# Performance work log

Hardware: AMD Instinct MI355X
Metric: run time of the kernel (lower is better)

Reference implementation:

```python
import jax, jax.numpy as jnp
import numpy as np

H = 12  # num_heads


def rotate_half(x):
    x1, x2 = jnp.split(x, 2, axis=-1)
    return jnp.concatenate([-x2, x1], axis=-1)


def setup_inputs() -> dict:
    key = jax.random.key(0)
    ks = jax.random.split(key, 8)
    B, N, C = 4, 2048, 768
    num_special = 5
    Ns = N - num_special
    D = C // H
    x = jax.random.normal(ks[0], (B, N, C), dtype=jnp.float32)
    rope_cos = jax.random.uniform(ks[1], (Ns, D), dtype=jnp.float32)
    rope_sin = jax.random.uniform(ks[2], (Ns, D), dtype=jnp.float32)
    W_qkv = jax.random.normal(ks[3], (C, 3 * C), dtype=jnp.float32) * (C ** -0.5)
    b_qkv = jax.random.normal(ks[4], (3 * C,), dtype=jnp.float32) * 0.02
    W_proj = jax.random.normal(ks[5], (C, C), dtype=jnp.float32) * (C ** -0.5)
    b_proj = jax.random.normal(ks[6], (C,), dtype=jnp.float32) * 0.02
    return {"x": x, "rope_cos": rope_cos, "rope_sin": rope_sin,
            "W_qkv": W_qkv, "b_qkv": b_qkv, "W_proj": W_proj, "b_proj": b_proj,
            "num_special": num_special}


def reference(x, rope_cos, rope_sin, W_qkv, b_qkv, W_proj, b_proj, num_special):
    B, N, C = x.shape
    D = C // H
    scale = D ** -0.5
    qkv = (x @ W_qkv + b_qkv).reshape(B, N, 3, H, D)
    qkv = jnp.transpose(qkv, (2, 0, 3, 1, 4))  # [3, B, H, N, D]
    q, k, v = qkv[0], qkv[1], qkv[2]
    # partial RoPE: special tokens untouched, spatial tokens rotated
    q_spec, q_spat = q[:, :, :num_special], q[:, :, num_special:]
    k_spec, k_spat = k[:, :, :num_special], k[:, :, num_special:]
    q_spat = q_spat * rope_cos + rotate_half(q_spat) * rope_sin
    k_spat = k_spat * rope_cos + rotate_half(k_spat) * rope_sin
    q = jnp.concatenate([q_spec, q_spat], axis=2)
    k = jnp.concatenate([k_spec, k_spat], axis=2)
    attn = jnp.einsum('bhqd,bhkd->bhqk', q, k) * scale  # [B,H,N,N]
    attn = jax.nn.softmax(attn, axis=-1)
    out = jnp.einsum('bhqk,bhkd->bhqd', attn, v)  # [B,H,N,D]
    out = jnp.transpose(out, (0, 2, 1, 3)).reshape(B, N, C)
    return out @ W_proj + b_proj
```

## Files before the change

kernel.cpp:

```cpp
#include <hip/hip_runtime.h>
#include <stdint.h>

typedef unsigned short u16;
typedef __bf16 bf16x8 __attribute__((ext_vector_type(8)));
typedef short s16x4 __attribute__((ext_vector_type(4)));
typedef float f32x4 __attribute__((ext_vector_type(4)));

typedef __attribute__((address_space(1))) void gvoid_t;
typedef __attribute__((address_space(3))) void lvoid_t;

struct alignas(16) U128 { uint32_t x, y, z, w; };
struct alignas(16) F128 { float x, y, z, w; };
struct alignas(8)  U64v { uint32_t x, y; };

__device__ __forceinline__ void gld16(const u16* g, u16* lds) {
  __builtin_amdgcn_global_load_lds((gvoid_t*)const_cast<u16*>(g),
                                   (lvoid_t*)lds, 16, 0, 0);
}

__device__ __forceinline__ u16 f2bf(float f) {
  uint32_t u = __builtin_bit_cast(uint32_t, f);
  u += 0x7FFFu + ((u >> 16) & 1u);
  return (u16)(u >> 16);
}
__device__ __forceinline__ float bf2f(u16 h) {
  return __builtin_bit_cast(float, (uint32_t)h << 16);
}
__device__ __forceinline__ bf16x8 ldfrag(const u16* p) {
  U128 u = *reinterpret_cast<const U128*>(p);
  return __builtin_bit_cast(bf16x8, u);
}
__device__ __forceinline__ uint32_t pkbf(float a, float b) {
  uint32_t ua = __builtin_bit_cast(uint32_t, a) + 0x8000u;
  uint32_t ub = __builtin_bit_cast(uint32_t, b) + 0x8000u;
  return (ua >> 16) | (ub & 0xFFFF0000u);
}

__device__ __forceinline__ float EXP2(float x) { return __builtin_amdgcn_exp2f(x); }

__global__ void cvt_f32_bf16(const float* __restrict__ in, u16* __restrict__ out) {
  int i = (blockIdx.x * 256 + threadIdx.x) * 4;
  F128 v = *reinterpret_cast<const F128*>(in + i);
  U64v o;
  o.x = (uint32_t)f2bf(v.x) | ((uint32_t)f2bf(v.y) << 16);
  o.y = (uint32_t)f2bf(v.z) | ((uint32_t)f2bf(v.w) << 16);
  *reinterpret_cast<U64v*>(out + i) = o;
}

__global__ void transpose_cvt(const float* __restrict__ W, u16* __restrict__ Wt,
                              int K, int N) {
  __shared__ float T[32][33];
  const int n0 = blockIdx.x * 32, k0 = blockIdx.y * 32;
  const int tid = threadIdx.x;
#pragma unroll
  for (int i = 0; i < 4; ++i) {
    int e = i * 256 + tid, r = e >> 5, c = e & 31;
    T[r][c] = W[(size_t)(k0 + r) * N + n0 + c];
  }
  __syncthreads();
#pragma unroll
  for (int i = 0; i < 4; ++i) {
    int e = i * 256 + tid, r = e >> 5, c = e & 31;
    Wt[(size_t)(n0 + r) * K + k0 + c] = f2bf(T[c][r]);
  }
}

__global__ __launch_bounds__(256, 2)
void gemm_bt(const u16* __restrict__ A, const u16* __restrict__ Bt,
             const float* __restrict__ bias, float* __restrict__ C,
             int M, int N, int K) {
  __shared__ u16 As[128 * 32];
  __shared__ u16 Bs[128 * 32];
  const int tid = threadIdx.x;
  const int wave = tid >> 6, lane = tid & 63;
  const int quad = lane >> 4, l16 = lane & 15;
  const int m0 = blockIdx.y * 128, n0 = blockIdx.x * 128;
  const int wr = (wave & 1) * 64, wc = (wave >> 1) * 64;

  f32x4 acc[4][4];
#pragma unroll
  for (int i = 0; i < 4; ++i)
#pragma unroll
    for (int j = 0; j < 4; ++j) acc[i][j] = (f32x4){0.f, 0.f, 0.f, 0.f};

  for (int k0 = 0; k0 < K; k0 += 32) {
    __syncthreads();
#pragma unroll
    for (int j = 0; j < 2; ++j) {
      int c = (wave * 2 + j) * 64 + lane;
      int row = c >> 2, kq = c & 3;
      gld16(A + (size_t)(m0 + row) * K + k0 + kq * 8, &As[(wave * 2 + j) * 512]);
      gld16(Bt + (size_t)(n0 + row) * K + k0 + kq * 8, &Bs[(wave * 2 + j) * 512]);
    }
    __syncthreads();
    bf16x8 af[4], bfr[4];
#pragma unroll
    for (int rb = 0; rb < 4; ++rb) af[rb] = ldfrag(&As[(wr + rb * 16 + l16) * 32 + quad * 8]);
#pragma unroll
    for (int cb = 0; cb < 4; ++cb) bfr[cb] = ldfrag(&Bs[(wc + cb * 16 + l16) * 32 + quad * 8]);
#pragma unroll
    for (int rb = 0; rb < 4; ++rb)
#pragma unroll
      for (int cb = 0; cb < 4; ++cb)
        acc[rb][cb] = __builtin_amdgcn_mfma_f32_16x16x32_bf16(af[rb], bfr[cb], acc[rb][cb], 0, 0, 0);
  }
#pragma unroll
  for (int cb = 0; cb < 4; ++cb) {
    int col = n0 + wc + cb * 16 + l16;
    float bv = bias[col];
#pragma unroll
    for (int rb = 0; rb < 4; ++rb) {
#pragma unroll
      for (int r = 0; r < 4; ++r) {
        int row = m0 + wr + rb * 16 + quad * 4 + r;
        C[(size_t)row * N + col] = acc[rb][cb][r] + bv;
      }
    }
  }
}

__global__ __launch_bounds__(256, 2)
void gemm_qkv_rope(const u16* __restrict__ A, const u16* __restrict__ Bt,
                   const float* __restrict__ bias,
                   const float* __restrict__ cosT, const float* __restrict__ sinT,
                   const int* __restrict__ nsp,
                   u16* __restrict__ Qo, u16* __restrict__ Ko, u16* __restrict__ Vto) {
  __shared__ u16 As[128 * 32];
  __shared__ u16 Bs[128 * 32];
  const int K = 768, N = 2304;
  const int tid = threadIdx.x;
  const int wave = tid >> 6, lane = tid & 63;
  const int quad = lane >> 4, l16 = lane & 15;
  const int m0 = blockIdx.y * 128, n0 = blockIdx.x * 128;
  const int wr = (wave & 1) * 64, wc = (wave >> 1) * 64;

  f32x4 acc[4][4];
#pragma unroll
  for (int i = 0; i < 4; ++i)
#pragma unroll
    for (int j = 0; j < 4; ++j) acc[i][j] = (f32x4){0.f, 0.f, 0.f, 0.f};

  for (int k0 = 0; k0 < K; k0 += 32) {
    __syncthreads();
#pragma unroll
    for (int j = 0; j < 2; ++j) {
      int c = (wave * 2 + j) * 64 + lane;
      int row = c >> 2, kq = c & 3;
      gld16(A + (size_t)(m0 + row) * K + k0 + kq * 8, &As[(wave * 2 + j) * 512]);
      gld16(Bt + (size_t)(n0 + row) * K + k0 + kq * 8, &Bs[(wave * 2 + j) * 512]);
    }
    __syncthreads();
    bf16x8 af[4], bfr[4];
#pragma unroll
    for (int rb = 0; rb < 4; ++rb) af[rb] = ldfrag(&As[(wr + rb * 16 + l16) * 32 + quad * 8]);
#pragma unroll
    for (int cb = 0; cb < 4; ++cb) bfr[cb] = ldfrag(&Bs[(wc + cb * 16 + l16) * 32 + quad * 8]);
#pragma unroll
    for (int rb = 0; rb < 4; ++rb)
#pragma unroll
      for (int cb = 0; cb < 4; ++cb)
        acc[rb][cb] = __builtin_amdgcn_mfma_f32_16x16x32_bf16(af[rb], bfr[cb], acc[rb][cb], 0, 0, 0);
  }

  const int sec = blockIdx.x / 6;
  const int gcol0 = n0 + wc;
  const int hh = (gcol0 >> 6) % 12;
  const int bb = m0 >> 11;
  const int nbase = m0 & 2047;
  const int bh = bb * 12 + hh;
  const int num_special = nsp[0];
  const float QS = 0.125f * 1.4426950408889634f;

  if (sec < 2) {
    u16* outp = sec ? Ko : Qo;
    const float qs = sec ? 1.0f : QS;
#pragma unroll
    for (int cbp = 0; cbp < 2; ++cbp) {
      const int d1 = cbp * 16 + l16;
      const int d2 = d1 + 32;
      const float bv1 = bias[gcol0 + d1];
      const float bv2 = bias[gcol0 + d2];
#pragma unroll
      for (int rb = 0; rb < 4; ++rb) {
#pragma unroll
        for (int r = 0; r < 4; ++r) {
          const int n = nbase + wr + rb * 16 + quad * 4 + r;
          float v1 = acc[rb][cbp][r] + bv1;
          float v2 = acc[rb][cbp + 2][r] + bv2;
          float o1, o2;
          if (n < num_special) {
            o1 = v1; o2 = v2;
          } else {
            int ns = n - num_special;
            float c1 = cosT[ns * 64 + d1], s1 = sinT[ns * 64 + d1];
            float c2 = cosT[ns * 64 + d2], s2 = sinT[ns * 64 + d2];
            o1 = v1 * c1 - v2 * s1;
            o2 = v2 * c2 + v1 * s2;
          }
          size_t ob = ((size_t)bh * 2048 + n) * 64;
          outp[ob + d1] = f2bf(o1 * qs);
          outp[ob + d2] = f2bf(o2 * qs);
        }
      }
    }
  } else {
#pragma unroll
    for (int cb = 0; cb < 4; ++cb) {
      const int d = cb * 16 + l16;
      const float bv = bias[gcol0 + d];
#pragma unroll
      for (int rb = 0; rb < 4; ++rb) {
        const int nr = nbase + wr + rb * 16 + quad * 4;
        U64v o;
        o.x = (uint32_t)f2bf(acc[rb][cb][0] + bv) |
              ((uint32_t)f2bf(acc[rb][cb][1] + bv) << 16);
        o.y = (uint32_t)f2bf(acc[rb][cb][2] + bv) |
              ((uint32_t)f2bf(acc[rb][cb][3] + bv) << 16);
        *(U64v*)&Vto[((size_t)bh * 64 + d) * 2048 + nr] = o;
      }
    }
  }
}

__global__ __launch_bounds__(256, 3)
void attn(const u16* __restrict__ Q, const u16* __restrict__ Kg,
          const u16* __restrict__ Vt, u16* __restrict__ Out) {
  __shared__ u16 smem[2 * 64 * 72];
  __shared__ float invS[64];
  u16* Ks = smem;
  u16* Vs = smem + 64 * 72;
  u16* Qs = smem;
  const int tid = threadIdx.x;
  const int wave = tid >> 6, lane = tid & 63;
  const int quad = lane >> 4, l16 = lane & 15;
  const int idx = blockIdx.x;
  const int bh = idx % 48, qt = idx / 48;
  const int b = bh / 12, h = bh % 12;
  const u16* Qb = Q + (size_t)bh * 2048 * 64;
  const u16* Kb = Kg + (size_t)bh * 2048 * 64;
  const u16* Vb = Vt + (size_t)bh * 64 * 2048;
  const int wkey0 = wave * 16;

#pragma unroll
  for (int j = 0; j < 2; ++j) {
    int c = j * 256 + tid;
    int row = c >> 3, kq = c & 7;
    *(U128*)&Qs[row * 72 + kq * 8] =
        *(const U128*)(Qb + (size_t)(qt * 64 + row) * 64 + kq * 8);
  }
  __syncthreads();
  bf16x8 qf[4][2];
#pragma unroll
  for (int m = 0; m < 4; ++m) {
    qf[m][0] = ldfrag(&Qs[(m * 16 + l16) * 72 + quad * 8]);
    qf[m][1] = ldfrag(&Qs[(m * 16 + l16) * 72 + quad * 8 + 32]);
  }

  f32x4 oacc[4][4];
#pragma unroll
  for (int m = 0; m < 4; ++m)
#pragma unroll
    for (int db = 0; db < 4; ++db) oacc[m][db] = (f32x4){0.f, 0.f, 0.f, 0.f};
  float psum[4] = {0.f, 0.f, 0.f, 0.f};

  for (int kt = 0; kt < 32; ++kt) {
    __syncthreads();
#pragma unroll
    for (int j = 0; j < 2; ++j) {
      int c = j * 256 + tid;
      int row = c >> 3, kq = c & 7;
      *(U128*)&Ks[row * 72 + kq * 8] =
          *(const U128*)(Kb + (size_t)(kt * 64 + row) * 64 + kq * 8);
      *(U128*)&Vs[row * 72 + kq * 8] =
          *(const U128*)(Vb + (size_t)row * 2048 + kt * 64 + kq * 8);
    }
    __syncthreads();

    bf16x8 ka0 = ldfrag(&Ks[(wkey0 + l16) * 72 + quad * 8]);
    bf16x8 ka1 = ldfrag(&Ks[(wkey0 + l16) * 72 + quad * 8 + 32]);

    s16x4 pf[4];
#pragma unroll
    for (int m = 0; m < 4; ++m) {
      f32x4 st = (f32x4){0.f, 0.f, 0.f, 0.f};
      st = __builtin_amdgcn_mfma_f32_16x16x32_bf16(ka0, qf[m][0], st, 0, 0, 0);
      st = __builtin_amdgcn_mfma_f32_16x16x32_bf16(ka1, qf[m][1], st, 0, 0, 0);
      float p0 = EXP2(st[0]);
      float p1 = EXP2(st[1]);
      float p2 = EXP2(st[2]);
      float p3 = EXP2(st[3]);
      psum[m] += (p0 + p1) + (p2 + p3);
      U64v pd;
      pd.x = pkbf(p0, p1);
      pd.y = pkbf(p2, p3);
      pf[m] = __builtin_bit_cast(s16x4, pd);
    }

#pragma unroll
    for (int db = 0; db < 4; ++db) {
      s16x4 vf = __builtin_bit_cast(s16x4,
          *(const U64v*)&Vs[(db * 16 + l16) * 72 + wkey0 + quad * 4]);
#pragma unroll
      for (int m = 0; m < 4; ++m)
        oacc[m][db] = __builtin_amdgcn_mfma_f32_16x16x16bf16_1k(pf[m], vf, oacc[m][db], 0, 0, 0);
    }
  }

#pragma unroll
  for (int m = 0; m < 4; ++m) {
    psum[m] += __shfl_xor(psum[m], 16, 64);
    psum[m] += __shfl_xor(psum[m], 32, 64);
  }
  __syncthreads();
  float* LS = (float*)smem;
  if (quad == 0) {
#pragma unroll
    for (int m = 0; m < 4; ++m) LS[wave * 64 + m * 16 + l16] = psum[m];
  }
  __syncthreads();
  if (tid < 64) {
    float tot = LS[tid] + LS[64 + tid] + LS[128 + tid] + LS[192 + tid];
    invS[tid] = 1.0f / tot;
  }

  float* OR = (float*)smem;
  const int q = tid >> 2;
  const int d0 = (tid & 3) * 4;
  const size_t obase = ((size_t)(b * 2048 + qt * 64 + q)) * 768 + h * 64 + d0;
#pragma unroll
  for (int db = 0; db < 4; ++db) {
    __syncthreads();
#pragma unroll
    for (int m = 0; m < 4; ++m)
#pragma unroll
      for (int r = 0; r < 4; ++r)
        OR[(wave * 64 + m * 16 + quad * 4 + r) * 18 + l16] = oacc[m][db][r];
    __syncthreads();
    float s0 = 0.f, s1 = 0.f, s2 = 0.f, s3 = 0.f;
#pragma unroll
    for (int w = 0; w < 4; ++w) {
      const float* p = &OR[(w * 64 + q) * 18 + d0];
      s0 += p[0]; s1 += p[1]; s2 += p[2]; s3 += p[3];
    }
    float iv = invS[q];
    U64v o;
    o.x = (uint32_t)f2bf(s0 * iv) | ((uint32_t)f2bf(s1 * iv) << 16);
    o.y = (uint32_t)f2bf(s2 * iv) | ((uint32_t)f2bf(s3 * iv) << 16);
    *(U64v*)&Out[obase + db * 16] = o;
  }
}

extern "C" void kernel_launch(void* const* d_in, const int* in_sizes, int n_in,
                              void* d_out, int out_size, void* d_ws, size_t ws_size,
                              hipStream_t stream) {
  (void)in_sizes; (void)n_in; (void)out_size; (void)ws_size;
  const float* x        = (const float*)d_in[0];
  const float* rope_cos = (const float*)d_in[1];
  const float* rope_sin = (const float*)d_in[2];
  const float* W_qkv    = (const float*)d_in[3];
  const float* b_qkv    = (const float*)d_in[4];
  const float* W_proj   = (const float*)d_in[5];
  const float* b_proj   = (const float*)d_in[6];
  const int*   nsp      = (const int*)d_in[7];
  float* out = (float*)d_out;

  char* ws = (char*)d_ws;
  u16* Xb   = (u16*)(ws);
  u16* Wqkt = (u16*)(ws + 12582912);
  u16* Wpt  = (u16*)(ws + 16121856);
  u16* Qb   = (u16*)(ws + 55050240);
  u16* Kb   = (u16*)(ws + 67633152);
  u16* Vtb  = (u16*)(ws + 80216064);
  u16* att  = (u16*)(ws + 92798976);

  cvt_f32_bf16<<<6144, 256, 0, stream>>>(x, Xb);
  transpose_cvt<<<dim3(72, 24), 256, 0, stream>>>(W_qkv, Wqkt, 768, 2304);
  transpose_cvt<<<dim3(24, 24), 256, 0, stream>>>(W_proj, Wpt, 768, 768);
  gemm_qkv_rope<<<dim3(18, 64), 256, 0, stream>>>(Xb, Wqkt, b_qkv, rope_cos, rope_sin,
                                                  nsp, Qb, Kb, Vtb);
  attn<<<1536, 256, 0, stream>>>(Qb, Kb, Vtb, att);
  gemm_bt<<<dim3(6, 64), 256, 0, stream>>>(att, Wpt, b_proj, out, 8192, 768, 768);
}
```

Baseline: 249.3 us.

## Double-buffer K/V tiles with async global-to-LDS loads and XOR swizzle

The attention kernel now keeps two K/V buffers in shared memory and prefetches the next key tile with global_load_lds while the current tile feeds the MFMAs. That removes one barrier per iteration and overlaps global loads with compute. The padded stride-72 layout is replaced by a 64-wide XOR-swizzled layout to avoid LDS bank conflicts without padding. Q is staged through one of the K buffers the same way. Shared memory per block grows to 32 KB, which may limit occupancy, and the correctness of the shared buffers depends on barrier ordering.

```diff
diff --git a/kernel.cpp b/kernel.cpp
--- a/kernel.cpp
+++ b/kernel.cpp
@@ -225,11 +225,12 @@
 __global__ __launch_bounds__(256, 3)
 void attn(const u16* __restrict__ Q, const u16* __restrict__ Kg,
           const u16* __restrict__ Vt, u16* __restrict__ Out) {
-  __shared__ u16 smem[2 * 64 * 72];
+  __shared__ u16 smem[4 * 4096];
   __shared__ float invS[64];
-  u16* Ks = smem;
-  u16* Vs = smem + 64 * 72;
-  u16* Qs = smem;
+  u16* K0 = smem;
+  u16* V0 = smem + 4096;
+  u16* K1 = smem + 8192;
+  u16* V1 = smem + 12288;
   const int tid = threadIdx.x;
   const int wave = tid >> 6, lane = tid & 63;
   const int quad = lane >> 4, l16 = lane & 15;
@@ -241,19 +242,29 @@
   const u16* Vb = Vt + (size_t)bh * 64 * 2048;
   const int wkey0 = wave * 16;
 
-#pragma unroll
-  for (int j = 0; j < 2; ++j) {
-    int c = j * 256 + tid;
-    int row = c >> 3, kq = c & 7;
-    *(U128*)&Qs[row * 72 + kq * 8] =
-        *(const U128*)(Qb + (size_t)(qt * 64 + row) * 64 + kq * 8);
-  }
+  const int srow = lane >> 3;
+  const int scol = (lane & 7) ^ srow;
+  const int row0 = wave * 16 + srow;
+  const int row1 = wave * 16 + 8 + srow;
+  const int dst0 = wave * 1024;
+  const int dst1 = wave * 1024 + 512;
+
+  gld16(Qb + (size_t)(qt * 64 + row0) * 64 + scol * 8, K1 + dst0);
+  gld16(Qb + (size_t)(qt * 64 + row1) * 64 + scol * 8, K1 + dst1);
+  gld16(Kb + row0 * 64 + scol * 8, K0 + dst0);
+  gld16(Kb + row1 * 64 + scol * 8, K0 + dst1);
+  gld16(Vb + (size_t)row0 * 2048 + scol * 8, V0 + dst0);
+  gld16(Vb + (size_t)row1 * 2048 + scol * 8, V0 + dst1);
   __syncthreads();
+
+  const int r7 = l16 & 7;
+  const int kc = quad ^ r7;
   bf16x8 qf[4][2];
 #pragma unroll
   for (int m = 0; m < 4; ++m) {
-    qf[m][0] = ldfrag(&Qs[(m * 16 + l16) * 72 + quad * 8]);
-    qf[m][1] = ldfrag(&Qs[(m * 16 + l16) * 72 + quad * 8 + 32]);
+    const u16* qrow = &K1[(m * 16 + l16) * 64];
+    qf[m][0] = ldfrag(qrow + kc * 8);
+    qf[m][1] = ldfrag(qrow + (kc ^ 4) * 8);
   }
 
   f32x4 oacc[4][4];
@@ -263,21 +274,26 @@
     for (int db = 0; db < 4; ++db) oacc[m][db] = (f32x4){0.f, 0.f, 0.f, 0.f};
   float psum[4] = {0.f, 0.f, 0.f, 0.f};
 
+  const int vchunk = wave * 2 + (quad >> 1);
+  const int voff = (quad & 1) * 4;
+
   for (int kt = 0; kt < 32; ++kt) {
     __syncthreads();
-#pragma unroll
-    for (int j = 0; j < 2; ++j) {
-      int c = j * 256 + tid;
-      int row = c >> 3, kq = c & 7;
-      *(U128*)&Ks[row * 72 + kq * 8] =
-          *(const U128*)(Kb + (size_t)(kt * 64 + row) * 64 + kq * 8);
-      *(U128*)&Vs[row * 72 + kq * 8] =
-          *(const U128*)(Vb + (size_t)row * 2048 + kt * 64 + kq * 8);
-    }
-    __syncthreads();
-
-    bf16x8 ka0 = ldfrag(&Ks[(wkey0 + l16) * 72 + quad * 8]);
-    bf16x8 ka1 = ldfrag(&Ks[(wkey0 + l16) * 72 + quad * 8 + 32]);
+    const u16* cK = (kt & 1) ? K1 : K0;
+    const u16* cV = (kt & 1) ? V1 : V0;
+    if (kt < 31) {
+      u16* nK = (kt & 1) ? K0 : K1;
+      u16* nV = (kt & 1) ? V0 : V1;
+      const int nk = kt + 1;
+      gld16(Kb + nk * 4096 + row0 * 64 + scol * 8, nK + dst0);
+      gld16(Kb + nk * 4096 + row1 * 64 + scol * 8, nK + dst1);
+      gld16(Vb + (size_t)row0 * 2048 + nk * 64 + scol * 8, nV + dst0);
+      gld16(Vb + (size_t)row1 * 2048 + nk * 64 + scol * 8, nV + dst1);
+    }
+
+    const u16* krow = &cK[(wkey0 + l16) * 64];
+    bf16x8 ka0 = ldfrag(krow + kc * 8);
+    bf16x8 ka1 = ldfrag(krow + (kc ^ 4) * 8);
 
     s16x4 pf[4];
 #pragma unroll
@@ -298,8 +314,9 @@
 
 #pragma unroll
     for (int db = 0; db < 4; ++db) {
+      const int vrow = db * 16 + l16;
       s16x4 vf = __builtin_bit_cast(s16x4,
-          *(const U64v*)&Vs[(db * 16 + l16) * 72 + wkey0 + quad * 4]);
+          *(const U64v*)&cV[vrow * 64 + (vchunk ^ r7) * 8 + voff]);
 #pragma unroll
       for (int m = 0; m < 4; ++m)
         oacc[m][db] = __builtin_amdgcn_mfma_f32_16x16x16bf16_1k(pf[m], vf, oacc[m][db], 0, 0, 0);
```

New measurement: 251.8 us. About the same (+1.0%).
